# Kernel tuning notes

Measured on AMD Instinct MI355X. Metric: run time of the kernel, lower is better.

The kernel has to match this reference:

```python
import jax, jax.numpy as jnp
import numpy as np

NUM_HEADS = 4
EPS = 1e-5


def conv1(W, b, z):
    # Conv1d with kernel_size=1 == channel-wise linear: (B, Cin, L) -> (B, Cout, L)
    return jnp.einsum('oi,bil->bol', W, z) + b[None, :, None]


def setup_inputs() -> dict:
    key = jax.random.key(0)
    ks = jax.random.split(key, 16)
    B, D, N = 2, 256, 4096
    s = 0.05
    return {
        'x': jax.random.normal(ks[0], (B, D, N), jnp.float32),
        'source': jax.random.normal(ks[1], (B, D, N), jnp.float32),
        'Wq': jax.random.normal(ks[2], (D, D), jnp.float32) * s,
        'bq': jax.random.normal(ks[3], (D,), jnp.float32) * s,
        'Wk': jax.random.normal(ks[4], (D, D), jnp.float32) * s,
        'bk': jax.random.normal(ks[5], (D,), jnp.float32) * s,
        'Wv': jax.random.normal(ks[6], (D, D), jnp.float32) * s,
        'bv': jax.random.normal(ks[7], (D,), jnp.float32) * s,
        'Wm': jax.random.normal(ks[8], (D, D), jnp.float32) * s,
        'bm': jax.random.normal(ks[9], (D,), jnp.float32) * s,
        'W1': jax.random.normal(ks[10], (2 * D, 2 * D), jnp.float32) * s,
        'b1': jax.random.normal(ks[11], (2 * D,), jnp.float32) * s,
        'W2': jax.random.normal(ks[12], (D, 2 * D), jnp.float32) * s,
        'b2': jax.random.normal(ks[13], (D,), jnp.float32) * s,
    }


def reference(x, source, Wq, bq, Wk, bk, Wv, bv, Wm, bm, W1, b1, W2, b2):
    B, D, N = x.shape
    M = source.shape[2]
    H = NUM_HEADS
    dim = D // H  # per-head dim; torch reshape splits channels as (dim, heads)

    q = conv1(Wq, bq, x).reshape(B, dim, H, N)
    k = conv1(Wk, bk, source).reshape(B, dim, H, M)
    v = conv1(Wv, bv, source).reshape(B, dim, H, M)

    scores = jnp.einsum('bdhn,bdhm->bhnm', q, k) / (dim ** 0.5)
    prob = jax.nn.softmax(scores, axis=-1)
    attn = jnp.einsum('bhnm,bdhm->bdhn', prob, v).reshape(B, D, N)

    message = conv1(Wm, bm, attn)

    h = conv1(W1, b1, jnp.concatenate([x, message], axis=1))
    # InstanceNorm1d (affine=False, biased var over L)
    mu = jnp.mean(h, axis=2, keepdims=True)
    var = jnp.mean((h - mu) ** 2, axis=2, keepdims=True)
    h = jax.nn.relu((h - mu) / jnp.sqrt(var + EPS))
    return conv1(W2, b2, h)
```

## Files before the change

kernel.cpp:

```cpp
#include <hip/hip_runtime.h>
#include <cstdint>
#include <cstddef>


typedef __attribute__((ext_vector_type(8))) short short8;
typedef __attribute__((ext_vector_type(4))) float floatx4;

union U4 { unsigned int u[4]; short8 s; };

__device__ __forceinline__ unsigned short f2bf(float x) {
  union { float f; unsigned int u; } c; c.f = x;
  unsigned int r = c.u + 0x7FFFu + ((c.u >> 16) & 1u);
  return (unsigned short)(r >> 16);
}
__device__ __forceinline__ float bf2f(unsigned short u) {
  union { unsigned int i; float f; } c; c.i = ((unsigned int)u) << 16; return c.f;
}
__device__ __forceinline__ void gload16(const void* g, void* l) {
  __builtin_amdgcn_global_load_lds(
      (const __attribute__((address_space(1))) unsigned int*)g,
      (__attribute__((address_space(3))) unsigned int*)l, 16, 0, 0);
}
__device__ __forceinline__ unsigned int cvtpk(float lo, float hi) {
  unsigned int r;
  asm("v_cvt_pk_bf16_f32 %0, %1, %2" : "=v"(r) : "v"(lo), "v"(hi));
  return r;
}

#define LOG2E_8 0.18033688011112042f

__global__ __launch_bounds__(256) void prep_all(
    const float* __restrict__ x, const float* __restrict__ src,
    unsigned short* __restrict__ xb, unsigned short* __restrict__ sb,
    const float* __restrict__ Wq, const float* __restrict__ Wk,
    const float* __restrict__ Wv, const float* __restrict__ Wm,
    const float* __restrict__ W1, const float* __restrict__ W2,
    const float* __restrict__ bq, const float* __restrict__ bk,
    const float* __restrict__ bv, const float* __restrict__ bm,
    const float* __restrict__ b1, const float* __restrict__ b2,
    unsigned short* __restrict__ wqkv, unsigned short* __restrict__ wmT,
    unsigned short* __restrict__ w1a, unsigned short* __restrict__ w1bb,
    unsigned short* __restrict__ w2_, float* __restrict__ biasb,
    float* __restrict__ bcb, int C, int N)
{
  const int t = threadIdx.x;
  if (blockIdx.x < 4096) {
    __shared__ float tile[32][33];
    const int tb = blockIdx.x;
    const int z = tb >> 10, rem = tb & 1023;
    const int bx = rem & 127, by = rem >> 7;
    const int which = z >> 1, b = z & 1;
    const float* X = which ? src : x;
    unsigned short* Y = which ? sb : xb;
    const int n0 = bx * 32, c0 = by * 32;
    const int tc = t & 31, tr = t >> 5;
    #pragma unroll
    for (int i = 0; i < 4; ++i)
      tile[tr + i * 8][tc] = X[((size_t)b * C + c0 + tr + i * 8) * N + n0 + tc];
    __syncthreads();
    #pragma unroll
    for (int i = 0; i < 4; ++i)
      Y[((size_t)b * N + n0 + tr + i * 8) * C + c0 + tc] = f2bf(tile[tc][tr + i * 8]);
    return;
  }
  const int bid = blockIdx.x - 4096;
  if (bid < 768) {
    const int idx = bid * 256 + t;
    const int op = idx >> 8, ip = idx & 255;
    const int grp = op >> 8, oo = op & 255;
    const int o = 4 * (oo & 63) + (oo >> 6);
    const float* W = grp == 0 ? Wq : grp == 1 ? Wk : Wv;
    const float sc = grp == 0 ? LOG2E_8 : 1.f;
    wqkv[idx] = f2bf(W[(size_t)o * 256 + ip] * sc);
  } else if (bid < 1024) {
    const int idx = (bid - 768) * 256 + t;
    const int hm = idx >> 8, c = idx & 255;
    const int ph = 4 * (hm & 63) + (hm >> 6);
    wmT[idx] = f2bf(Wm[(size_t)c * 256 + ph]);
  } else if (bid < 1536) {
    const int idx = (bid - 1024) * 256 + t;
    const int o = idx >> 8, c = idx & 255;
    w1a[idx] = f2bf(W1[(size_t)o * 512 + c]);
  } else if (bid < 2048) {
    const int idx = (bid - 1536) * 256 + t;
    const int o = idx >> 8, c = idx & 255;
    w1bb[idx] = f2bf(W1[(size_t)o * 512 + 256 + c]);
  } else if (bid < 2560) {
    const int idx = (bid - 2048) * 256 + t;
    w2_[idx] = f2bf(W2[idx]);
  } else if (bid < 2566) {
    const int z = (bid - 2560) * 256 + t;
    if (z < 256)       biasb[z] = bq[4 * (z & 63) + (z >> 6)] * LOG2E_8;
    else if (z < 512)  { const int y = z - 256; biasb[z] = bk[4 * (y & 63) + (y >> 6)]; }
    else if (z < 768)  { const int y = z - 512; biasb[z] = bv[4 * (y & 63) + (y >> 6)]; }
    else if (z < 1280) biasb[z] = 0.f;
    else if (z < 1536) biasb[z] = b2[z - 1280];
  } else {
    const int o = (bid - 2566) * 256 + t;
    float a = b1[o];
    for (int c = 0; c < 256; ++c)
      a += W1[(size_t)o * 512 + 256 + c] * bm[c];
    bcb[o] = a;
  }
}

__global__ __launch_bounds__(256) void gemm128(
    const unsigned short* __restrict__ W0, const unsigned short* __restrict__ W1p,
    const float* __restrict__ bias,
    const unsigned short* __restrict__ X0, const unsigned short* __restrict__ X1,
    void* __restrict__ O0, void* __restrict__ O1, void* __restrict__ O2,
    int Co, int Ci, int Ci0, int Wci0, int N, int variant)
{
  const int n0 = blockIdx.x * 128;
  const int o0 = blockIdx.y * 128;
  const int b  = blockIdx.z;
  const int t  = threadIdx.x;
  const int w = t >> 6, lane = t & 63, qd = lane >> 4, l = lane & 15;
  const int oh = (w >> 1) * 64, nh = (w & 1) * 64;

  __shared__ unsigned short Wl[128 * 64];
  __shared__ unsigned short Xl[128 * 64];

  floatx4 acc[4][4];
  #pragma unroll
  for (int i = 0; i < 4; ++i)
    #pragma unroll
    for (int j = 0; j < 4; ++j) acc[i][j] = (floatx4){0.f, 0.f, 0.f, 0.f};

  for (int k0 = 0; k0 < Ci; k0 += 64) {
    const unsigned short* Xs; int cb, rl;
    if (variant == 1) { Xs = (o0 < 256) ? X0 : X1; cb = k0; rl = Ci; }
    else if (k0 < Ci0) { Xs = X0; cb = k0; rl = Ci0; }
    else               { Xs = X1; cb = k0 - Ci0; rl = Ci - Ci0; }
    const unsigned short* Ws; int wb, wrl;
    if (k0 < Wci0) { Ws = W0; wb = k0; wrl = Wci0; }
    else           { Ws = W1p; wb = k0 - Wci0; wrl = Ci - Wci0; }
    __syncthreads();
    #pragma unroll
    for (int i = 0; i < 4; ++i) {
      const int idx = i * 256 + t;
      const int row = idx >> 3, pg = idx & 7, sg = pg ^ (row & 7);
      gload16(&Ws[(size_t)(o0 + row) * wrl + wb + sg * 8], &Wl[row * 64 + pg * 8]);
      gload16(&Xs[((size_t)b * N + n0 + row) * rl + cb + sg * 8], &Xl[row * 64 + pg * 8]);
    }
    __syncthreads();

    short8 af[4][2], bf[4][2];
    #pragma unroll
    for (int i = 0; i < 4; ++i) {
      const int ar = oh + 16 * i + l;
      af[i][0] = *(const short8*)&Wl[ar * 64 + ((qd ^ (ar & 7))) * 8];
      af[i][1] = *(const short8*)&Wl[ar * 64 + (((4 + qd) ^ (ar & 7))) * 8];
    }
    #pragma unroll
    for (int j = 0; j < 4; ++j) {
      const int br = nh + 16 * j + l;
      bf[j][0] = *(const short8*)&Xl[br * 64 + ((qd ^ (br & 7))) * 8];
      bf[j][1] = *(const short8*)&Xl[br * 64 + (((4 + qd) ^ (br & 7))) * 8];
    }
    #pragma unroll
    for (int i = 0; i < 4; ++i)
      #pragma unroll
      for (int j = 0; j < 4; ++j) {
        acc[i][j] = __builtin_amdgcn_mfma_f32_16x16x32_bf16(af[i][0], bf[j][0], acc[i][j], 0, 0, 0);
        acc[i][j] = __builtin_amdgcn_mfma_f32_16x16x32_bf16(af[i][1], bf[j][1], acc[i][j], 0, 0, 0);
      }
  }

  const int osec = o0 + oh;
  #pragma unroll
  for (int i = 0; i < 4; ++i) {
    const int o4 = o0 + oh + 16 * i + qd * 4;
    const float4 bi = *(const float4*)&bias[o4];
    #pragma unroll
    for (int j = 0; j < 4; ++j) {
      const int n = n0 + nh + 16 * j + l;
      if (variant == 0) {
        unsigned short* C = (unsigned short*)O0;
        ushort4 pk;
        pk.x = f2bf(acc[i][j][0] + bi.x); pk.y = f2bf(acc[i][j][1] + bi.y);
        pk.z = f2bf(acc[i][j][2] + bi.z); pk.w = f2bf(acc[i][j][3] + bi.w);
        *(ushort4*)&C[((size_t)b * N + n) * Co + o4] = pk;
      } else if (variant == 1) {
        if (osec < 256) {
          unsigned short* C = (unsigned short*)O0;
          ushort4 pk;
          pk.x = f2bf(acc[i][j][0] + bi.x); pk.y = f2bf(acc[i][j][1] + bi.y);
          pk.z = f2bf(acc[i][j][2] + bi.z); pk.w = f2bf(acc[i][j][3] + bi.w);
          *(ushort4*)&C[((size_t)b * N + n) * 256 + o4] = pk;
        } else if (osec < 512) {
          unsigned short* C = (unsigned short*)O1;
          ushort4 pk;
          pk.x = f2bf(acc[i][j][0] + bi.x); pk.y = f2bf(acc[i][j][1] + bi.y);
          pk.z = f2bf(acc[i][j][2] + bi.z); pk.w = f2bf(acc[i][j][3] + bi.w);
          *(ushort4*)&C[((size_t)b * N + n) * 256 + (o4 - 256)] = pk;
        } else {
          unsigned short* C = (unsigned short*)O2;
          #pragma unroll
          for (int rg = 0; rg < 4; ++rg) {
            const int op = o4 - 512 + rg, h = op >> 6, d = op & 63;
            C[(((size_t)b * 4 + h) * 64 + d) * N + n] =
                f2bf(acc[i][j][rg] + ((const float*)&bi)[rg]);
          }
        }
      } else if (variant == 2) {
        float* C = (float*)O0;
        #pragma unroll
        for (int rg = 0; rg < 4; ++rg)
          C[((size_t)b * Co + o4 + rg) * N + n] = acc[i][j][rg] + ((const float*)&bi)[rg];
      } else {
        unsigned short* C = (unsigned short*)O0;
        #pragma unroll
        for (int rg = 0; rg < 4; ++rg)
          C[(size_t)(o4 + rg) * N + n] = f2bf(acc[i][j][rg] + ((const float*)&bi)[rg]);
      }
    }
  }
}

__global__ __launch_bounds__(256) void attn_mfma(
    const unsigned short* __restrict__ qb, const unsigned short* __restrict__ kb,
    const unsigned short* __restrict__ vh, unsigned short* __restrict__ Opart,
    float* __restrict__ liPart, int N)
{
  const int qt = blockIdx.x;
  const int h  = blockIdx.y;
  const int b  = blockIdx.z >> 2, s = blockIdx.z & 3;
  const int n0 = qt * 128;
  const int t  = threadIdx.x;
  const int w = t >> 6, lane = t & 63, qd = lane >> 4, l = lane & 15;

  __shared__ unsigned short Kl[2][64 * 64];
  __shared__ unsigned short Vl[2][64 * 64];

  const unsigned short* qp0 = &qb[((size_t)b * N + n0 + 16 * w + l) * 256 + h * 64];
  const unsigned short* qp1 = qp0 + (size_t)64 * 256;
  short8 bQ[2][2];
  bQ[0][0] = *(const short8*)&qp0[qd * 8];
  bQ[0][1] = *(const short8*)&qp0[32 + qd * 8];
  bQ[1][0] = *(const short8*)&qp1[qd * 8];
  bQ[1][1] = *(const short8*)&qp1[32 + qd * 8];

  short8 ones;
  #pragma unroll
  for (int i = 0; i < 8; ++i) ones[i] = (short)0x3F80;

  floatx4 accO[2][4];
  floatx4 accLi[2];
  #pragma unroll
  for (int qs = 0; qs < 2; ++qs) {
    accLi[qs] = (floatx4){0.f, 0.f, 0.f, 0.f};
    #pragma unroll
    for (int ds = 0; ds < 4; ++ds) accO[qs][ds] = (floatx4){0.f, 0.f, 0.f, 0.f};
  }

  const int j0base = s * 1024;

  auto STAGE = [&](int buf, int j0) {
    #pragma unroll
    for (int i = 0; i < 2; ++i) {
      const int idx = i * 256 + t;
      const int row = idx >> 3, pg = idx & 7, sg = pg ^ (row & 7);
      gload16(&kb[((size_t)b * N + j0 + row) * 256 + h * 64 + sg * 8],
              &Kl[buf][row * 64 + pg * 8]);
      gload16(&vh[(((size_t)b * 4 + h) * 64 + row) * N + j0 + sg * 8],
              &Vl[buf][row * 64 + pg * 8]);
    }
  };

  STAGE(0, j0base);

  #pragma unroll 2
  for (int jt = 0; jt < 16; ++jt) {
    const int cur = jt & 1;
    __syncthreads();
    if (jt < 15) STAGE(cur ^ 1, j0base + (jt + 1) * 64);

    floatx4 S[2][4];
    __builtin_amdgcn_s_setprio(1);
    #pragma unroll
    for (int js = 0; js < 4; ++js) {
      const int br = 16 * js + l;
      const short8 k0 = *(const short8*)&Kl[cur][br * 64 + ((qd ^ (br & 7))) * 8];
      const short8 k1 = *(const short8*)&Kl[cur][br * 64 + (((4 + qd) ^ (br & 7))) * 8];
      floatx4 a0 = (floatx4){0.f, 0.f, 0.f, 0.f};
      floatx4 a1 = (floatx4){0.f, 0.f, 0.f, 0.f};
      a0 = __builtin_amdgcn_mfma_f32_16x16x32_bf16(k0, bQ[0][0], a0, 0, 0, 0);
      a1 = __builtin_amdgcn_mfma_f32_16x16x32_bf16(k0, bQ[1][0], a1, 0, 0, 0);
      a0 = __builtin_amdgcn_mfma_f32_16x16x32_bf16(k1, bQ[0][1], a0, 0, 0, 0);
      a1 = __builtin_amdgcn_mfma_f32_16x16x32_bf16(k1, bQ[1][1], a1, 0, 0, 0);
      S[0][js] = a0; S[1][js] = a1;
    }
    __builtin_amdgcn_s_setprio(0);

    unsigned int T[2][2][4];
    #pragma unroll
    for (int qs = 0; qs < 2; ++qs) {
      unsigned int U[4], W[4];
      #pragma unroll
      for (int js = 0; js < 4; ++js) {
        const float p0 = __builtin_exp2f(S[qs][js][0]);
        const float p1 = __builtin_exp2f(S[qs][js][1]);
        const float p2 = __builtin_exp2f(S[qs][js][2]);
        const float p3 = __builtin_exp2f(S[qs][js][3]);
        U[js] = cvtpk(p0, p1);
        W[js] = cvtpk(p2, p3);
      }
      #pragma unroll
      for (int js2 = 0; js2 < 2; ++js2) {
        unsigned int t0 = U[2 * js2], t2 = U[2 * js2 + 1];
        asm("v_permlane32_swap_b32 %0, %1" : "+v"(t0), "+v"(t2));
        asm("v_permlane16_swap_b32 %0, %1" : "+v"(t0), "+v"(t2));
        unsigned int t1 = W[2 * js2], t3 = W[2 * js2 + 1];
        asm("v_permlane32_swap_b32 %0, %1" : "+v"(t1), "+v"(t3));
        asm("v_permlane16_swap_b32 %0, %1" : "+v"(t1), "+v"(t3));
        T[qs][js2][0] = t0; T[qs][js2][1] = t1;
        T[qs][js2][2] = t2; T[qs][js2][3] = t3;
      }
    }

    __builtin_amdgcn_s_setprio(1);
    #pragma unroll
    for (int js2 = 0; js2 < 2; ++js2) {
      short8 vv[4];
      #pragma unroll
      for (int ds = 0; ds < 4; ++ds) {
        const int vr = 16 * ds + l;
        vv[ds] = *(const short8*)&Vl[cur][vr * 64 + (((4 * js2 + qd) ^ (vr & 7))) * 8];
      }
      #pragma unroll
      for (int qs = 0; qs < 2; ++qs) {
        U4 pu;
        pu.u[0] = T[qs][js2][0]; pu.u[1] = T[qs][js2][1];
        pu.u[2] = T[qs][js2][2]; pu.u[3] = T[qs][js2][3];
        const short8 pa = pu.s;
        #pragma unroll
        for (int ds = 0; ds < 4; ++ds)
          accO[qs][ds] = __builtin_amdgcn_mfma_f32_16x16x32_bf16(pa, vv[ds], accO[qs][ds], 0, 0, 0);
        accLi[qs] = __builtin_amdgcn_mfma_f32_16x16x32_bf16(pa, ones, accLi[qs], 0, 0, 0);
      }
    }
    __builtin_amdgcn_s_setprio(0);
  }

  const size_t obase = ((((size_t)b * 4 + h) * 4 + s) * 32 + qt) * 128;
  #pragma unroll
  for (int qs = 0; qs < 2; ++qs)
    #pragma unroll
    for (int rg = 0; rg < 4; ++rg) {
      const int q = qs * 64 + 16 * w + qd * 4 + rg;
      #pragma unroll
      for (int ds = 0; ds < 4; ++ds)
        Opart[(obase + q) * 64 + 16 * ds + l] = f2bf(accO[qs][ds][rg]);
      if (l == 0) liPart[obase + q] = accLi[qs][rg];
    }
}

__global__ __launch_bounds__(256) void attn_combine(
    const unsigned short* __restrict__ Opart, const float* __restrict__ liPart,
    unsigned short* __restrict__ atb, int N)
{
  const int qt = blockIdx.x, h = blockIdx.y, b = blockIdx.z;
  const int t = threadIdx.x;
  const int q = t >> 1, d0 = (t & 1) * 32;

  float li = 0.f;
  size_t idx[4];
  #pragma unroll
  for (int s = 0; s < 4; ++s) {
    idx[s] = ((((size_t)b * 4 + h) * 4 + s) * 32 + qt) * 128 + q;
    li += liPart[idx[s]];
  }
  const float inv = 1.f / li;

  float o[32];
  #pragma unroll
  for (int c = 0; c < 32; ++c) o[c] = 0.f;
  #pragma unroll
  for (int s = 0; s < 4; ++s) {
    #pragma unroll
    for (int c4 = 0; c4 < 4; ++c4) {
      const short8 v = *(const short8*)&Opart[idx[s] * 64 + d0 + c4 * 8];
      #pragma unroll
      for (int j = 0; j < 8; ++j) o[c4 * 8 + j] += bf2f((unsigned short)v[j]);
    }
  }
  unsigned short* dst = &atb[((size_t)b * N + qt * 128 + q) * 256 + h * 64 + d0];
  #pragma unroll
  for (int c4 = 0; c4 < 4; ++c4) {
    ushort4 pk;
    pk.x = f2bf(o[c4 * 8 + 0] * inv); pk.y = f2bf(o[c4 * 8 + 1] * inv);
    pk.z = f2bf(o[c4 * 8 + 2] * inv); pk.w = f2bf(o[c4 * 8 + 3] * inv);
    *(ushort4*)&dst[c4 * 8] = pk;
    pk.x = f2bf(o[c4 * 8 + 4] * inv); pk.y = f2bf(o[c4 * 8 + 5] * inv);
    pk.z = f2bf(o[c4 * 8 + 6] * inv); pk.w = f2bf(o[c4 * 8 + 7] * inv);
    *(ushort4*)&dst[c4 * 8 + 4] = pk;
  }
}

__global__ __launch_bounds__(256) void in_stats(
    const unsigned short* __restrict__ H, float* __restrict__ Ps,
    float* __restrict__ Ps2, int N)
{
  const int cg = blockIdx.x, ns = blockIdx.y, b = blockIdx.z, t = threadIdx.x;
  const int c0 = cg * 64 + (t & 7) * 8;
  float s[8] = {}, s2[8] = {};
  #pragma unroll
  for (int i = 0; i < 8; ++i) {
    const int n = ns * 256 + (t >> 3) + i * 32;
    const short8 hv = *(const short8*)&H[((size_t)b * N + n) * 512 + c0];
    #pragma unroll
    for (int j = 0; j < 8; ++j) {
      const float f = bf2f((unsigned short)hv[j]);
      s[j] += f; s2[j] += f * f;
    }
  }
  __shared__ float rs[32][64], rs2[32][64];
  #pragma unroll
  for (int j = 0; j < 8; ++j) {
    rs[t >> 3][(t & 7) * 8 + j] = s[j];
    rs2[t >> 3][(t & 7) * 8 + j] = s2[j];
  }
  __syncthreads();
  if (t < 64) {
    float a = 0.f, a2 = 0.f;
    #pragma unroll
    for (int r = 0; r < 32; ++r) { a += rs[r][t]; a2 += rs2[r][t]; }
    const size_t o = ((size_t)ns * 2 + b) * 512 + cg * 64 + t;
    Ps[o] = a; Ps2[o] = a2;
  }
}

__global__ __launch_bounds__(256) void in_norm(
    unsigned short* __restrict__ H, const float* __restrict__ Ps,
    const float* __restrict__ Ps2, int N)
{
  const int cg = blockIdx.x, ns = blockIdx.y, b = blockIdx.z, t = threadIdx.x;
  __shared__ float muS[64], ivS[64];
  if (t < 64) {
    const int c = cg * 64 + t;
    float s = 0.f, s2 = 0.f;
    for (int k = 0; k < 16; ++k) {
      s  += Ps [((size_t)k * 2 + b) * 512 + c];
      s2 += Ps2[((size_t)k * 2 + b) * 512 + c];
    }
    const float mu = s / (float)N;
    const float var = fmaxf(s2 / (float)N - mu * mu, 0.f);
    muS[t] = mu;
    ivS[t] = rsqrtf(var + 1e-5f);
  }
  __syncthreads();
  const int c0 = cg * 64 + (t & 7) * 8;
  float mu[8], iv[8];
  #pragma unroll
  for (int j = 0; j < 8; ++j) {
    mu[j] = muS[(t & 7) * 8 + j];
    iv[j] = ivS[(t & 7) * 8 + j];
  }
  #pragma unroll
  for (int i = 0; i < 8; ++i) {
    const int n = ns * 256 + (t >> 3) + i * 32;
    unsigned short* p = &H[((size_t)b * N + n) * 512 + c0];
    short8 hv = *(const short8*)p;
    #pragma unroll
    for (int j = 0; j < 8; ++j) {
      const float f = fmaxf((bf2f((unsigned short)hv[j]) - mu[j]) * iv[j], 0.f);
      hv[j] = (short)f2bf(f);
    }
    *(short8*)p = hv;
  }
}

extern "C" void kernel_launch(void* const* d_in, const int* in_sizes, int n_in,
                              void* d_out, int out_size, void* d_ws, size_t ws_size,
                              hipStream_t stream)
{
  const int B = 2, D = 256, N = 4096;

  const float* x   = (const float*)d_in[0];
  const float* src = (const float*)d_in[1];
  const float* Wq  = (const float*)d_in[2];  const float* bq = (const float*)d_in[3];
  const float* Wk  = (const float*)d_in[4];  const float* bk = (const float*)d_in[5];
  const float* Wv  = (const float*)d_in[6];  const float* bv = (const float*)d_in[7];
  const float* Wm  = (const float*)d_in[8];  const float* bm = (const float*)d_in[9];
  const float* W1  = (const float*)d_in[10]; const float* b1 = (const float*)d_in[11];
  const float* W2  = (const float*)d_in[12]; const float* b2 = (const float*)d_in[13];
  float* out = (float*)d_out;

  char* ws = (char*)d_ws;
  const size_t MB = 1u << 20;
  unsigned short* xb  = (unsigned short*)(ws + 0 * MB);
  unsigned short* sb  = (unsigned short*)(ws + 4 * MB);
  unsigned short* qbf = (unsigned short*)(ws + 8 * MB);
  unsigned short* kbf = (unsigned short*)(ws + 12 * MB);
  unsigned short* vhb = (unsigned short*)(ws + 16 * MB);
  unsigned short* atb = (unsigned short*)(ws + 20 * MB);
  unsigned short* Opart = (unsigned short*)(ws + 24 * MB);
  unsigned short* hb  = (unsigned short*)(ws + 28 * MB);
  float* liPart = (float*)(ws + 41 * MB);
  unsigned short* wqkvb = (unsigned short*)(ws + 42 * MB);
  unsigned short* wmT  = wqkvb + 768 * 256;
  unsigned short* w1a  = wmT + 256 * 256;
  unsigned short* w1bb = w1a + 512 * 256;
  unsigned short* w2b  = w1bb + 512 * 256;
  unsigned short* wcb  = w2b + 256 * 512;
  float* biasb = (float*)(ws + 44 * MB);
  float* bcb   = biasb + 1536;
  float* Ps    = biasb + 2048;
  float* Ps2   = Ps + 16 * 2 * 512;

  const dim3 blk(256);

  prep_all<<<dim3(4096 + 2568), blk, 0, stream>>>(
      x, src, xb, sb, Wq, Wk, Wv, Wm, W1, W2,
      bq, bk, bv, bm, b1, b2, wqkvb, wmT, w1a, w1bb, w2b, biasb, bcb, D, N);

  gemm128<<<dim3(2, 4, 1), blk, 0, stream>>>(
      w1bb, w1bb, biasb + 768 , wmT, wmT,
      wcb, nullptr, nullptr, 512, 256, 256, 256, 256, 3);

  gemm128<<<dim3(N / 128, 6, B), blk, 0, stream>>>(
      wqkvb, wqkvb, biasb, xb, sb, qbf, kbf, vhb, 768, 256, 256, 256, N, 1);

  attn_mfma<<<dim3(N / 128, 4, B * 4), blk, 0, stream>>>(
      qbf, kbf, vhb, Opart, liPart, N);
  attn_combine<<<dim3(N / 128, 4, B), blk, 0, stream>>>(Opart, liPart, atb, N);

  gemm128<<<dim3(N / 128, 4, B), blk, 0, stream>>>(
      w1a, wcb, bcb, xb, atb, hb, nullptr, nullptr, 512, 512, 256, 256, N, 0);

  in_stats<<<dim3(8, 16, B), blk, 0, stream>>>(hb, Ps, Ps2, N);
  in_norm<<<dim3(8, 16, B), blk, 0, stream>>>(hb, Ps, Ps2, N);

  gemm128<<<dim3(N / 128, 2, B), blk, 0, stream>>>(
      w2b, w2b, biasb + 1280, hb, hb, out, nullptr, nullptr, 256, 512, 512, 512, N, 2);
}
```

Measured before the change: 226.3 us.

## Read K/V directly from global memory in attention and remap blocks per XCD

The attention kernel drops its double-buffered LDS staging of K and V tiles and the per-tile barriers. Each wave now loads its K and V fragments straight from global memory, relying on L2 caching. The grid is flattened to 1D with (batch, head) chosen by block id modulo 8, so all blocks for one head land on the same XCD and share its L2. This removes LDS traffic and synchronisation, but every wave now issues redundant global loads and there is no prefetch to hide memory latency.

```diff
diff --git a/kernel.cpp b/kernel.cpp
--- a/kernel.cpp
+++ b/kernel.cpp
@@ -223,15 +223,14 @@
     const unsigned short* __restrict__ vh, unsigned short* __restrict__ Opart,
     float* __restrict__ liPart, int N)
 {
-  const int qt = blockIdx.x;
-  const int h  = blockIdx.y;
-  const int b  = blockIdx.z >> 2, s = blockIdx.z & 3;
+  const int bid = blockIdx.x;
+  const int xcd = bid & 7;
+  const int b = xcd >> 2, h = xcd & 3;
+  const int inner = bid >> 3;
+  const int qt = inner & 31, s = inner >> 5;
   const int n0 = qt * 128;
   const int t  = threadIdx.x;
   const int w = t >> 6, lane = t & 63, qd = lane >> 4, l = lane & 15;
-
-  __shared__ unsigned short Kl[2][64 * 64];
-  __shared__ unsigned short Vl[2][64 * 64];
 
   const unsigned short* qp0 = &qb[((size_t)b * N + n0 + 16 * w + l) * 256 + h * 64];
   const unsigned short* qp1 = qp0 + (size_t)64 * 256;
@@ -254,35 +253,21 @@
     for (int ds = 0; ds < 4; ++ds) accO[qs][ds] = (floatx4){0.f, 0.f, 0.f, 0.f};
   }
 
+  const unsigned short* kbase = &kb[(size_t)b * N * 256 + h * 64];
+  const unsigned short* vbase = &vh[((size_t)b * 4 + h) * 64 * (size_t)N];
+
   const int j0base = s * 1024;
 
-  auto STAGE = [&](int buf, int j0) {
-    #pragma unroll
-    for (int i = 0; i < 2; ++i) {
-      const int idx = i * 256 + t;
-      const int row = idx >> 3, pg = idx & 7, sg = pg ^ (row & 7);
-      gload16(&kb[((size_t)b * N + j0 + row) * 256 + h * 64 + sg * 8],
-              &Kl[buf][row * 64 + pg * 8]);
-      gload16(&vh[(((size_t)b * 4 + h) * 64 + row) * N + j0 + sg * 8],
-              &Vl[buf][row * 64 + pg * 8]);
-    }
-  };
-
-  STAGE(0, j0base);
-
-  #pragma unroll 2
   for (int jt = 0; jt < 16; ++jt) {
-    const int cur = jt & 1;
-    __syncthreads();
-    if (jt < 15) STAGE(cur ^ 1, j0base + (jt + 1) * 64);
+    const int j0 = j0base + jt * 64;
 
     floatx4 S[2][4];
     __builtin_amdgcn_s_setprio(1);
     #pragma unroll
     for (int js = 0; js < 4; ++js) {
-      const int br = 16 * js + l;
-      const short8 k0 = *(const short8*)&Kl[cur][br * 64 + ((qd ^ (br & 7))) * 8];
-      const short8 k1 = *(const short8*)&Kl[cur][br * 64 + (((4 + qd) ^ (br & 7))) * 8];
+      const int key = j0 + 16 * js + l;
+      const short8 k0 = *(const short8*)&kbase[(size_t)key * 256 + qd * 8];
+      const short8 k1 = *(const short8*)&kbase[(size_t)key * 256 + 32 + qd * 8];
       floatx4 a0 = (floatx4){0.f, 0.f, 0.f, 0.f};
       floatx4 a1 = (floatx4){0.f, 0.f, 0.f, 0.f};
       a0 = __builtin_amdgcn_mfma_f32_16x16x32_bf16(k0, bQ[0][0], a0, 0, 0, 0);
@@ -326,7 +311,7 @@
       #pragma unroll
       for (int ds = 0; ds < 4; ++ds) {
         const int vr = 16 * ds + l;
-        vv[ds] = *(const short8*)&Vl[cur][vr * 64 + (((4 * js2 + qd) ^ (vr & 7))) * 8];
+        vv[ds] = *(const short8*)&vbase[(size_t)vr * N + j0 + js2 * 32 + qd * 8];
       }
       #pragma unroll
       for (int qs = 0; qs < 2; ++qs) {
@@ -522,7 +507,7 @@
   gemm128<<<dim3(N / 128, 6, B), blk, 0, stream>>>(
       wqkvb, wqkvb, biasb, xb, sb, qbf, kbf, vhb, 768, 256, 256, 256, N, 1);
 
-  attn_mfma<<<dim3(N / 128, 4, B * 4), blk, 0, stream>>>(
+  attn_mfma<<<dim3(1024), blk, 0, stream>>>(
       qbf, kbf, vhb, Opart, liPart, N);
   attn_combine<<<dim3(N / 128, 4, B), blk, 0, stream>>>(Opart, liPart, atb, N);
 
```

Result: slower. 299.4 us (+32.3%).

## Fuse instance-norm statistics into GEMM epilogue and fold Wc precompute into prep

Applied to the files above, without the earlier changes.

Computes the per-channel sum and sum-of-squares for instance norm inside the h-producing GEMM epilogue, using wave shuffles and global atomics, and drops the separate in_stats kernel. The fused W1b·Wm weight is now computed in fp32 inside prep_all instead of by a separate tiny GEMM launch, and the accumulators are zeroed there too. This removes two kernel launches and one full read of h, at the cost of atomic contention and extra epilogue ALU work in the GEMM.

```diff
diff --git a/kernel.cpp b/kernel.cpp
--- a/kernel.cpp
+++ b/kernel.cpp
@@ -38,10 +38,10 @@
     const float* __restrict__ bq, const float* __restrict__ bk,
     const float* __restrict__ bv, const float* __restrict__ bm,
     const float* __restrict__ b1, const float* __restrict__ b2,
-    unsigned short* __restrict__ wqkv, unsigned short* __restrict__ wmT,
-    unsigned short* __restrict__ w1a, unsigned short* __restrict__ w1bb,
-    unsigned short* __restrict__ w2_, float* __restrict__ biasb,
-    float* __restrict__ bcb, int C, int N)
+    unsigned short* __restrict__ wqkv, unsigned short* __restrict__ w1a,
+    unsigned short* __restrict__ w2_, unsigned short* __restrict__ wcb,
+    float* __restrict__ biasb, float* __restrict__ bcb,
+    float* __restrict__ Ps, float* __restrict__ Ps2, int C, int N)
 {
   const int t = threadIdx.x;
   if (blockIdx.x < 4096) {
@@ -72,35 +72,46 @@
     const float* W = grp == 0 ? Wq : grp == 1 ? Wk : Wv;
     const float sc = grp == 0 ? LOG2E_8 : 1.f;
     wqkv[idx] = f2bf(W[(size_t)o * 256 + ip] * sc);
-  } else if (bid < 1024) {
+  } else if (bid < 1280) {
     const int idx = (bid - 768) * 256 + t;
-    const int hm = idx >> 8, c = idx & 255;
-    const int ph = 4 * (hm & 63) + (hm >> 6);
-    wmT[idx] = f2bf(Wm[(size_t)c * 256 + ph]);
-  } else if (bid < 1536) {
-    const int idx = (bid - 1024) * 256 + t;
     const int o = idx >> 8, c = idx & 255;
     w1a[idx] = f2bf(W1[(size_t)o * 512 + c]);
-  } else if (bid < 2048) {
-    const int idx = (bid - 1536) * 256 + t;
-    const int o = idx >> 8, c = idx & 255;
-    w1bb[idx] = f2bf(W1[(size_t)o * 512 + 256 + c]);
-  } else if (bid < 2560) {
-    const int idx = (bid - 2048) * 256 + t;
+  } else if (bid < 1792) {
+    const int idx = (bid - 1280) * 256 + t;
     w2_[idx] = f2bf(W2[idx]);
-  } else if (bid < 2566) {
-    const int z = (bid - 2560) * 256 + t;
+  } else if (bid < 1856) {
+    const int k = bid - 1792;
+    const int o0w = k * 8;
+    const int hm = 64 * (t & 3) + (t >> 2);
+    float acc[8] = {};
+    for (int c = 0; c < 256; ++c) {
+      const float wmv = Wm[(size_t)c * 256 + t];
+      #pragma unroll
+      for (int r = 0; r < 8; ++r)
+        acc[r] += W1[(size_t)(o0w + r) * 512 + 256 + c] * wmv;
+    }
+    #pragma unroll
+    for (int r = 0; r < 8; ++r)
+      wcb[(size_t)(o0w + r) * 256 + hm] = f2bf(acc[r]);
+  } else if (bid < 1862) {
+    const int z = (bid - 1856) * 256 + t;
     if (z < 256)       biasb[z] = bq[4 * (z & 63) + (z >> 6)] * LOG2E_8;
     else if (z < 512)  { const int y = z - 256; biasb[z] = bk[4 * (y & 63) + (y >> 6)]; }
     else if (z < 768)  { const int y = z - 512; biasb[z] = bv[4 * (y & 63) + (y >> 6)]; }
     else if (z < 1280) biasb[z] = 0.f;
     else if (z < 1536) biasb[z] = b2[z - 1280];
-  } else {
-    const int o = (bid - 2566) * 256 + t;
+  } else if (bid < 1864) {
+    const int o = (bid - 1862) * 256 + t;
     float a = b1[o];
     for (int c = 0; c < 256; ++c)
       a += W1[(size_t)o * 512 + 256 + c] * bm[c];
     bcb[o] = a;
+  } else {
+    #pragma unroll
+    for (int k = 0; k < 4; ++k) {
+      Ps[k * 256 + t] = 0.f;
+      Ps2[k * 256 + t] = 0.f;
+    }
   }
 }
 
@@ -109,6 +120,7 @@
     const float* __restrict__ bias,
     const unsigned short* __restrict__ X0, const unsigned short* __restrict__ X1,
     void* __restrict__ O0, void* __restrict__ O1, void* __restrict__ O2,
+    float* __restrict__ Ps, float* __restrict__ Ps2,
     int Co, int Ci, int Ci0, int Wci0, int N, int variant)
 {
   const int n0 = blockIdx.x * 128;
@@ -167,6 +179,12 @@
       }
   }
 
+  float sA[4][4], s2A[4][4];
+  #pragma unroll
+  for (int i = 0; i < 4; ++i)
+    #pragma unroll
+    for (int rg = 0; rg < 4; ++rg) { sA[i][rg] = 0.f; s2A[i][rg] = 0.f; }
+
   const int osec = o0 + oh;
   #pragma unroll
   for (int i = 0; i < 4; ++i) {
@@ -181,6 +199,14 @@
         pk.x = f2bf(acc[i][j][0] + bi.x); pk.y = f2bf(acc[i][j][1] + bi.y);
         pk.z = f2bf(acc[i][j][2] + bi.z); pk.w = f2bf(acc[i][j][3] + bi.w);
         *(ushort4*)&C[((size_t)b * N + n) * Co + o4] = pk;
+        if (Ps) {
+          const float v0 = bf2f(pk.x), v1 = bf2f(pk.y);
+          const float v2 = bf2f(pk.z), v3 = bf2f(pk.w);
+          sA[i][0] += v0; s2A[i][0] += v0 * v0;
+          sA[i][1] += v1; s2A[i][1] += v1 * v1;
+          sA[i][2] += v2; s2A[i][2] += v2 * v2;
+          sA[i][3] += v3; s2A[i][3] += v3 * v3;
+        }
       } else if (variant == 1) {
         if (osec < 256) {
           unsigned short* C = (unsigned short*)O0;
@@ -203,18 +229,31 @@
                 f2bf(acc[i][j][rg] + ((const float*)&bi)[rg]);
           }
         }
-      } else if (variant == 2) {
+      } else {
         float* C = (float*)O0;
         #pragma unroll
         for (int rg = 0; rg < 4; ++rg)
           C[((size_t)b * Co + o4 + rg) * N + n] = acc[i][j][rg] + ((const float*)&bi)[rg];
-      } else {
-        unsigned short* C = (unsigned short*)O0;
-        #pragma unroll
-        for (int rg = 0; rg < 4; ++rg)
-          C[(size_t)(o4 + rg) * N + n] = f2bf(acc[i][j][rg] + ((const float*)&bi)[rg]);
-      }
-    }
+      }
+    }
+  }
+
+  if (variant == 0 && Ps) {
+    #pragma unroll
+    for (int i = 0; i < 4; ++i)
+      #pragma unroll
+      for (int rg = 0; rg < 4; ++rg) {
+        float s = sA[i][rg], s2 = s2A[i][rg];
+        s += __shfl_xor(s, 1); s += __shfl_xor(s, 2);
+        s += __shfl_xor(s, 4); s += __shfl_xor(s, 8);
+        s2 += __shfl_xor(s2, 1); s2 += __shfl_xor(s2, 2);
+        s2 += __shfl_xor(s2, 4); s2 += __shfl_xor(s2, 8);
+        if (l == 0) {
+          const int c = o0 + oh + 16 * i + qd * 4 + rg;
+          atomicAdd(&Ps[(size_t)b * Co + c], s);
+          atomicAdd(&Ps2[(size_t)b * Co + c], s2);
+        }
+      }
   }
 }
 
@@ -398,39 +437,6 @@
   }
 }
 
-__global__ __launch_bounds__(256) void in_stats(
-    const unsigned short* __restrict__ H, float* __restrict__ Ps,
-    float* __restrict__ Ps2, int N)
-{
-  const int cg = blockIdx.x, ns = blockIdx.y, b = blockIdx.z, t = threadIdx.x;
-  const int c0 = cg * 64 + (t & 7) * 8;
-  float s[8] = {}, s2[8] = {};
-  #pragma unroll
-  for (int i = 0; i < 8; ++i) {
-    const int n = ns * 256 + (t >> 3) + i * 32;
-    const short8 hv = *(const short8*)&H[((size_t)b * N + n) * 512 + c0];
-    #pragma unroll
-    for (int j = 0; j < 8; ++j) {
-      const float f = bf2f((unsigned short)hv[j]);
-      s[j] += f; s2[j] += f * f;
-    }
-  }
-  __shared__ float rs[32][64], rs2[32][64];
-  #pragma unroll
-  for (int j = 0; j < 8; ++j) {
-    rs[t >> 3][(t & 7) * 8 + j] = s[j];
-    rs2[t >> 3][(t & 7) * 8 + j] = s2[j];
-  }
-  __syncthreads();
-  if (t < 64) {
-    float a = 0.f, a2 = 0.f;
-    #pragma unroll
-    for (int r = 0; r < 32; ++r) { a += rs[r][t]; a2 += rs2[r][t]; }
-    const size_t o = ((size_t)ns * 2 + b) * 512 + cg * 64 + t;
-    Ps[o] = a; Ps2[o] = a2;
-  }
-}
-
 __global__ __launch_bounds__(256) void in_norm(
     unsigned short* __restrict__ H, const float* __restrict__ Ps,
     const float* __restrict__ Ps2, int N)
@@ -439,11 +445,8 @@
   __shared__ float muS[64], ivS[64];
   if (t < 64) {
     const int c = cg * 64 + t;
-    float s = 0.f, s2 = 0.f;
-    for (int k = 0; k < 16; ++k) {
-      s  += Ps [((size_t)k * 2 + b) * 512 + c];
-      s2 += Ps2[((size_t)k * 2 + b) * 512 + c];
-    }
+    const float s  = Ps [(size_t)b * 512 + c];
+    const float s2 = Ps2[(size_t)b * 512 + c];
     const float mu = s / (float)N;
     const float var = fmaxf(s2 / (float)N - mu * mu, 0.f);
     muS[t] = mu;
@@ -499,39 +502,35 @@
   unsigned short* hb  = (unsigned short*)(ws + 28 * MB);
   float* liPart = (float*)(ws + 41 * MB);
   unsigned short* wqkvb = (unsigned short*)(ws + 42 * MB);
-  unsigned short* wmT  = wqkvb + 768 * 256;
-  unsigned short* w1a  = wmT + 256 * 256;
-  unsigned short* w1bb = w1a + 512 * 256;
-  unsigned short* w2b  = w1bb + 512 * 256;
+  unsigned short* w1a  = wqkvb + 768 * 256;
+  unsigned short* w2b  = w1a + 512 * 256;
   unsigned short* wcb  = w2b + 256 * 512;
   float* biasb = (float*)(ws + 44 * MB);
   float* bcb   = biasb + 1536;
   float* Ps    = biasb + 2048;
-  float* Ps2   = Ps + 16 * 2 * 512;
+  float* Ps2   = Ps + 1024;
 
   const dim3 blk(256);
 
-  prep_all<<<dim3(4096 + 2568), blk, 0, stream>>>(
+  prep_all<<<dim3(4096 + 1865), blk, 0, stream>>>(
       x, src, xb, sb, Wq, Wk, Wv, Wm, W1, W2,
-      bq, bk, bv, bm, b1, b2, wqkvb, wmT, w1a, w1bb, w2b, biasb, bcb, D, N);
-
-  gemm128<<<dim3(2, 4, 1), blk, 0, stream>>>(
-      w1bb, w1bb, biasb + 768 , wmT, wmT,
-      wcb, nullptr, nullptr, 512, 256, 256, 256, 256, 3);
+      bq, bk, bv, bm, b1, b2, wqkvb, w1a, w2b, wcb, biasb, bcb, Ps, Ps2, D, N);
 
   gemm128<<<dim3(N / 128, 6, B), blk, 0, stream>>>(
-      wqkvb, wqkvb, biasb, xb, sb, qbf, kbf, vhb, 768, 256, 256, 256, N, 1);
+      wqkvb, wqkvb, biasb, xb, sb, qbf, kbf, vhb, nullptr, nullptr,
+      768, 256, 256, 256, N, 1);
 
   attn_mfma<<<dim3(N / 128, 4, B * 4), blk, 0, stream>>>(
       qbf, kbf, vhb, Opart, liPart, N);
   attn_combine<<<dim3(N / 128, 4, B), blk, 0, stream>>>(Opart, liPart, atb, N);
 
   gemm128<<<dim3(N / 128, 4, B), blk, 0, stream>>>(
-      w1a, wcb, bcb, xb, atb, hb, nullptr, nullptr, 512, 512, 256, 256, N, 0);
-
-  in_stats<<<dim3(8, 16, B), blk, 0, stream>>>(hb, Ps, Ps2, N);
+      w1a, wcb, bcb, xb, atb, hb, nullptr, nullptr, Ps, Ps2,
+      512, 512, 256, 256, N, 0);
+
   in_norm<<<dim3(8, 16, B), blk, 0, stream>>>(hb, Ps, Ps2, N);
 
   gemm128<<<dim3(N / 128, 2, B), blk, 0, stream>>>(
-      w2b, w2b, biasb + 1280, hb, hb, out, nullptr, nullptr, 256, 512, 512, 512, N, 2);
-}
+      w2b, w2b, biasb + 1280, hb, hb, out, nullptr, nullptr, nullptr, nullptr,
+      256, 512, 512, 512, N, 2);
+}
```

Result: slower. 234.8 us (+3.8%).
